# Performance work log

Hardware: AMD Instinct MI355X
Metric: run time of the kernel (lower is better)

The kernel has to match this reference:

```python
import jax, jax.numpy as jnp
import numpy as np

E = 64; H = 4; DQK = 1; B = 2; R = 1225; C = 512; EPS_LN = 1e-5


def _ln(x, g, b):
    m = x.mean(-1, keepdims=True)
    v = jnp.mean((x - m) ** 2, -1, keepdims=True)
    return (x - m) / jnp.sqrt(v + EPS_LN) * g + b


def _lin_attn(x, wq, bq, wk, bk, wv, bv, wo, bo):
    # x: (b, r, c, e); attention over axis c (nb_col), per head, ELU+1 feature map
    b_, r_, c_, e_ = x.shape
    dv = e_ // H
    q = (x @ wq.T + bq).reshape(b_, r_, c_, H, DQK).swapaxes(2, 3)  # (b,r,H,c,dqk)
    k = (x @ wk.T + bk).reshape(b_, r_, c_, H, DQK).swapaxes(2, 3)
    v = (x @ wv.T + bv).reshape(b_, r_, c_, H, dv).swapaxes(2, 3)   # (b,r,H,c,dv)
    q = jax.nn.elu(q) + 1.0
    k = jax.nn.elu(k) + 1.0
    q = q / q.mean(axis=3, keepdims=True)  # mean over seq (c)
    k = k / k.sum(axis=3, keepdims=True)   # sum over seq (c)
    ktv = jnp.einsum('brhcd,brhce->brhde', k, v)   # (b,r,H,dqk,dv)
    o = jnp.einsum('brhcd,brhde->brhce', q, ktv)   # (b,r,H,c,dv)
    o = o.swapaxes(2, 3).reshape(b_, r_, c_, e_)
    return o @ wo.T + bo


def setup_inputs():
    key = jax.random.key(0)
    ks = iter(jax.random.split(key, 32))
    def w(shape, s=0.05):
        return jax.random.normal(next(ks), shape, jnp.float32) * s
    inp = {"x": jax.random.normal(next(ks), (B, E, R, C), jnp.float32)}
    for p in ("row", "col"):
        inp[p + "_wq"] = w((H, E)); inp[p + "_bq"] = jnp.zeros((H,), jnp.float32)
        inp[p + "_wk"] = w((H, E)); inp[p + "_bk"] = jnp.zeros((H,), jnp.float32)
        inp[p + "_wv"] = w((E, E)); inp[p + "_bv"] = jnp.zeros((E,), jnp.float32)
        inp[p + "_wo"] = w((E, E)); inp[p + "_bo"] = jnp.zeros((E,), jnp.float32)
    for p in ("rn", "cn", "fn"):
        inp[p + "_g"] = jnp.ones((E,), jnp.float32)
        inp[p + "_b"] = jnp.zeros((E,), jnp.float32)
    inp["w1"] = w((4 * E, E)); inp["b1"] = jnp.zeros((4 * E,), jnp.float32)
    inp["w2"] = w((E, 4 * E)); inp["b2"] = jnp.zeros((E,), jnp.float32)
    return inp


def reference(x, row_wq, row_bq, row_wk, row_bk, row_wv, row_bv, row_wo, row_bo,
              col_wq, col_bq, col_wk, col_bk, col_wv, col_bv, col_wo, col_bo,
              rn_g, rn_b, cn_g, cn_b, fn_g, fn_b, w1, b1, w2, b2):
    xe = jnp.moveaxis(x, 1, -1)  # (B, R, C, E)
    # row attention: attend over cols (C)
    h = xe + _lin_attn(_ln(xe, rn_g, rn_b),
                       row_wq, row_bq, row_wk, row_bk, row_wv, row_bv, row_wo, row_bo)
    # col attention: attend over rows (R) -> swap axes
    hc = _ln(h.swapaxes(1, 2), cn_g, cn_b)  # (B, C, R, E)
    h = h + _lin_attn(hc, col_wq, col_bq, col_wk, col_bk, col_wv, col_bv, col_wo, col_bo).swapaxes(1, 2)
    # 1x1-conv FFN == per-position MLP with exact GELU
    f = _ln(h, fn_g, fn_b)
    f = jax.nn.gelu(f @ w1.T + b1, approximate=False) @ w2.T + b2
    return jnp.moveaxis(h + f, -1, 1)  # (B, E, R, C)
```

## Files before the change

kernel.cpp:

```cpp
#include <hip/hip_runtime.h>
#include <cmath>

#define E_ 64
#define H_ 4
#define B_ 2
#define R_ 1225
#define C_ 512
#define EPS 1e-5f

__device__ __forceinline__ float elu1(float a) { return a > 0.f ? a + 1.f : __expf(a); }

typedef float f32x4 __attribute__((ext_vector_type(4)));
typedef short bf16x8 __attribute__((ext_vector_type(8)));
typedef short bf16x4 __attribute__((ext_vector_type(4)));

__device__ __forceinline__ unsigned short f2bf(float f) {
    union { float f; unsigned u; } c; c.f = f;
    unsigned u = c.u + 0x7FFFu + ((c.u >> 16) & 1u);
    return (unsigned short)(u >> 16);
}

__device__ __forceinline__ unsigned short f2bf_rn(float f) {
    union { float f; unsigned u; } c; c.f = f;
    return (unsigned short)((c.u + 0x8000u) >> 16);
}

__device__ __forceinline__ float bf2f(unsigned short s) {
    union { unsigned u; float f; } c; c.u = ((unsigned)s) << 16;
    return c.f;
}

__device__ __forceinline__ float gelu_fast(float a) {
    const float u = a * (-1.5957691216057308f - 0.0713548162726009f * a * a);
    return a / (1.f + __expf(u));
}


#define SXR 520

__global__ __launch_bounds__(512, 2) void row_attn(
    const float* __restrict__ x,
    const float* __restrict__ wq, const float* __restrict__ bq,
    const float* __restrict__ wk, const float* __restrict__ bk,
    const float* __restrict__ wv, const float* __restrict__ bv,
    const float* __restrict__ wo, const float* __restrict__ bo,
    const float* __restrict__ lng, const float* __restrict__ lnb,
    short* __restrict__ hout)
{
    const int r = blockIdx.x;
    const int b = blockIdx.y;
    const int t = threadIdx.x;
    const int w = t >> 6;
    const int l = t & 63;
    const int lr = l & 15;
    const int lq = l >> 4;

    __shared__ short s_xT[E_][SXR];
    __shared__ short s_kb[4][SXR];
    __shared__ float s_upart[2][H_][E_];
    __shared__ float s_ktv[E_];
    __shared__ float s_wok[E_][H_];
    __shared__ float s_qm[H_];
    __shared__ float s_sk[H_];
    __shared__ float s_S1[H_];
    __shared__ float red_q[8][H_];
    __shared__ float red_k[8][H_];
    __shared__ float red_k2[8][H_];
    __shared__ float s_cst[16];

    if (t < 16) {
        const int h = t & 3;
        const int kind = t >> 2;
        const float* wm = (kind < 2) ? wq : wk;
        const float* vm = (kind & 1) ? lnb : lng;
        float acc = 0.f;
        for (int e = 0; e < E_; ++e) acc += wm[h * E_ + e] * vm[e];
        s_cst[t] = acc;
    }
    __syncthreads();

    const size_t RC = (size_t)R_ * C_;
    const float* xbase = x + (size_t)b * E_ * RC + (size_t)r * C_;

    float qs[H_];
    float aq[H_], ak[H_], ak2[H_];
    {
        const float* xp = xbase + t;
        float s = 0.f, ss = 0.f;
        float dq[H_] = {0.f, 0.f, 0.f, 0.f};
        float dk[H_] = {0.f, 0.f, 0.f, 0.f};
        #pragma unroll 16
        for (int e = 0; e < E_; ++e) {
            const float xv = xp[(size_t)e * RC];
            s += xv; ss += xv * xv;
            const float t1 = lng[e] * xv;
            #pragma unroll
            for (int h = 0; h < H_; ++h) { dq[h] += wq[h * E_ + e] * t1; dk[h] += wk[h * E_ + e] * t1; }
            s_xT[e][t] = (short)f2bf(xv);
        }
        const float mu = s * (1.f / E_);
        const float rstd = rsqrtf(ss * (1.f / E_) - mu * mu + EPS);
        const float mr = mu * rstd;
        #pragma unroll
        for (int h = 0; h < H_; ++h) {
            const float qv = elu1(rstd * dq[h] - mr * s_cst[h]     + s_cst[4 + h]  + bq[h]);
            const float kv = elu1(rstd * dk[h] - mr * s_cst[8 + h] + s_cst[12 + h] + bk[h]);
            qs[h] = qv;
            aq[h] = qv; ak[h] = kv; ak2[h] = kv * mr;
            s_kb[h][t] = (short)f2bf(kv * rstd);
        }
    }
    __syncthreads();

    {
        const int et = w & 3;
        const int kh = w >> 2;
        f32x4 uacc; uacc[0] = uacc[1] = uacc[2] = uacc[3] = 0.f;
        #pragma unroll
        for (int ks = 0; ks < 8; ++ks) {
            const int co = kh * 256 + ks * 32 + lq * 8;
            bf16x8 af;
            #pragma unroll
            for (int i = 0; i < 8; ++i) af[i] = 0;
            if (lr < 4) af = *reinterpret_cast<const bf16x8*>(&s_kb[lr][co]);
            const bf16x8 bf = *reinterpret_cast<const bf16x8*>(&s_xT[et * 16 + lr][co]);
            uacc = __builtin_amdgcn_mfma_f32_16x16x32_bf16(af, bf, uacc, 0, 0, 0);
        }
        if (lq == 0) {
            #pragma unroll
            for (int i = 0; i < 4; ++i) s_upart[kh][i][et * 16 + lr] = uacc[i];
        }
    }

    #pragma unroll
    for (int h = 0; h < H_; ++h) {
        #pragma unroll
        for (int off = 32; off; off >>= 1) {
            aq[h] += __shfl_xor(aq[h], off, 64);
            ak[h] += __shfl_xor(ak[h], off, 64);
            ak2[h] += __shfl_xor(ak2[h], off, 64);
        }
    }
    if (l == 0) {
        #pragma unroll
        for (int h = 0; h < H_; ++h) { red_q[w][h] = aq[h]; red_k[w][h] = ak[h]; red_k2[w][h] = ak2[h]; }
    }
    __syncthreads();
    if (t < H_) {
        float sq = 0.f, sk = 0.f, s1 = 0.f;
        #pragma unroll
        for (int w2 = 0; w2 < 8; ++w2) { sq += red_q[w2][t]; sk += red_k[w2][t]; s1 += red_k2[w2][t]; }
        s_qm[t] = sq * (1.f / C_);
        s_sk[t] = sk;
        s_S1[t] = s1;
    }
    __syncthreads();
    if (t < H_ * E_) {
        const int h = t >> 6, e = t & 63;
        const float m1 = s_upart[0][h][e] + s_upart[1][h][e];
        s_upart[0][h][e] = lng[e] * (m1 - s_S1[h]) + lnb[e] * s_sk[h];
    }
    __syncthreads();
    if (t < E_) {
        const int h = t >> 4;
        float acc = 0.f;
        #pragma unroll
        for (int e = 0; e < E_; ++e) acc += wv[t * E_ + e] * s_upart[0][h][e];
        s_ktv[t] = acc / s_sk[h] + bv[t];
    }
    __syncthreads();
    if (t < E_) {
        #pragma unroll
        for (int h = 0; h < H_; ++h) {
            float acc = 0.f;
            #pragma unroll
            for (int d = 0; d < 16; ++d) acc += wo[t * E_ + h * 16 + d] * s_ktv[h * 16 + d];
            s_wok[t][h] = acc;
        }
    }
    __syncthreads();

    {
        float qn[H_];
        #pragma unroll
        for (int h = 0; h < H_; ++h) qn[h] = qs[h] / s_qm[h];
        short* hp = hout + ((size_t)((size_t)b * R_ + r) * C_ + t) * E_;
        #pragma unroll
        for (int e8 = 0; e8 < 8; ++e8) {
            bf16x8 o;
            #pragma unroll
            for (int i = 0; i < 8; ++i) {
                const int e = e8 * 8 + i;
                float tt = bo[e];
                #pragma unroll
                for (int h = 0; h < H_; ++h) tt += qn[h] * s_wok[e][h];
                o[i] = (short)f2bf(bf2f((unsigned short)s_xT[e][t]) + tt);
            }
            *reinterpret_cast<bf16x8*>(hp + e8 * 8) = o;
        }
    }
}

#define SX 264

__global__ __launch_bounds__(256, 3) void col_stats(
    const short* __restrict__ hbuf,
    const float* __restrict__ wq, const float* __restrict__ bq,
    const float* __restrict__ wk, const float* __restrict__ bk,
    const float* __restrict__ wv, const float* __restrict__ bv,
    const float* __restrict__ wo,
    const float* __restrict__ lng, const float* __restrict__ lnb,
    unsigned short* __restrict__ qbuf, float* __restrict__ wokq)
{
    const int c = blockIdx.x;
    const int b = blockIdx.y;
    const int t = threadIdx.x;
    const int w = t >> 6;
    const int l = t & 63;
    const int lr = l & 15;
    const int lq = l >> 4;

    __shared__ short s_xT[E_][SX];
    __shared__ short s_kb[4][SX];
    __shared__ float s_u[H_][E_];
    __shared__ float s_ktv[E_];
    __shared__ float s_wok[E_][H_];
    __shared__ float s_qm[H_];
    __shared__ float s_sk[H_];
    __shared__ float s_S1[H_];
    __shared__ float red_q[4][H_];
    __shared__ float red_k[4][H_];
    __shared__ float red_k2[4][H_];
    __shared__ float s_cst[16];

    if (t < 16) {
        const int h = t & 3;
        const int kind = t >> 2;
        const float* wm = (kind < 2) ? wq : wk;
        const float* vm = (kind & 1) ? lnb : lng;
        float acc = 0.f;
        for (int e = 0; e < E_; ++e) acc += wm[h * E_ + e] * vm[e];
        s_cst[t] = acc;
    }
    __syncthreads();

    const size_t CE = (size_t)C_ * E_;
    const short* hp0 = hbuf + (size_t)b * R_ * CE + (size_t)c * E_;
    unsigned short* qb0 = qbuf + ((size_t)(b * C_ + c)) * R_ * 4;

    float aq[H_]  = {0.f, 0.f, 0.f, 0.f};
    float ak[H_]  = {0.f, 0.f, 0.f, 0.f};
    float ak2[H_] = {0.f, 0.f, 0.f, 0.f};
    f32x4 uacc; uacc[0] = uacc[1] = uacc[2] = uacc[3] = 0.f;

    #pragma unroll 1
    for (int it = 0; it < 5; ++it) {
        const int rr = it * 256 + t;
        if (rr < R_) {
            const short* pp = hp0 + (size_t)rr * CE;
            bf16x8 hv8[8];
            #pragma unroll
            for (int g = 0; g < 8; ++g) hv8[g] = *reinterpret_cast<const bf16x8*>(pp + g * 8);
            float s = 0.f, ss = 0.f;
            float dq[H_] = {0.f, 0.f, 0.f, 0.f};
            float dk[H_] = {0.f, 0.f, 0.f, 0.f};
            #pragma unroll
            for (int g = 0; g < 8; ++g) {
                #pragma unroll
                for (int i = 0; i < 8; ++i) {
                    const int e = g * 8 + i;
                    const float xv = bf2f((unsigned short)hv8[g][i]);
                    s += xv; ss += xv * xv;
                    const float t1 = lng[e] * xv;
                    #pragma unroll
                    for (int h = 0; h < H_; ++h) { dq[h] += wq[h * E_ + e] * t1; dk[h] += wk[h * E_ + e] * t1; }
                    s_xT[e][t] = hv8[g][i];
                }
            }
            const float mu = s * (1.f / E_);
            const float rstd = rsqrtf(ss * (1.f / E_) - mu * mu + EPS);
            const float mr = mu * rstd;
            float qv[H_];
            #pragma unroll
            for (int h = 0; h < H_; ++h) {
                qv[h] = elu1(rstd * dq[h] - mr * s_cst[h]     + s_cst[4 + h]  + bq[h]);
                const float kv = elu1(rstd * dk[h] - mr * s_cst[8 + h] + s_cst[12 + h] + bk[h]);
                aq[h] += qv[h]; ak[h] += kv; ak2[h] += kv * mr;
                s_kb[h][t] = (short)f2bf(kv * rstd);
            }
            uint2 qp;
            qp.x = ((unsigned)f2bf(qv[1]) << 16) | f2bf(qv[0]);
            qp.y = ((unsigned)f2bf(qv[3]) << 16) | f2bf(qv[2]);
            *reinterpret_cast<uint2*>(qb0 + (size_t)rr * 4) = qp;
        } else {
            #pragma unroll
            for (int e = 0; e < E_; ++e) s_xT[e][t] = 0;
            #pragma unroll
            for (int h = 0; h < H_; ++h) s_kb[h][t] = 0;
        }
        __syncthreads();
        #pragma unroll
        for (int ks = 0; ks < 8; ++ks) {
            bf16x8 af;
            #pragma unroll
            for (int i = 0; i < 8; ++i) af[i] = 0;
            if (lr < 4) af = *reinterpret_cast<const bf16x8*>(&s_kb[lr][ks * 32 + lq * 8]);
            const bf16x8 bf = *reinterpret_cast<const bf16x8*>(&s_xT[w * 16 + lr][ks * 32 + lq * 8]);
            uacc = __builtin_amdgcn_mfma_f32_16x16x32_bf16(af, bf, uacc, 0, 0, 0);
        }
        __syncthreads();
    }

    #pragma unroll
    for (int h = 0; h < H_; ++h) {
        #pragma unroll
        for (int off = 32; off; off >>= 1) {
            aq[h] += __shfl_xor(aq[h], off, 64);
            ak[h] += __shfl_xor(ak[h], off, 64);
            ak2[h] += __shfl_xor(ak2[h], off, 64);
        }
    }
    if (l == 0) {
        #pragma unroll
        for (int h = 0; h < H_; ++h) { red_q[w][h] = aq[h]; red_k[w][h] = ak[h]; red_k2[w][h] = ak2[h]; }
    }
    __syncthreads();
    if (t < H_) {
        float sq = 0.f, sk = 0.f, s1 = 0.f;
        #pragma unroll
        for (int w2 = 0; w2 < 4; ++w2) { sq += red_q[w2][t]; sk += red_k[w2][t]; s1 += red_k2[w2][t]; }
        s_qm[t] = sq * (1.f / R_);
        s_sk[t] = sk;
        s_S1[t] = s1;
    }
    __syncthreads();
    if (lq == 0) {
        const int e = w * 16 + lr;
        #pragma unroll
        for (int i = 0; i < 4; ++i)
            s_u[i][e] = lng[e] * (uacc[i] - s_S1[i]) + lnb[e] * s_sk[i];
    }
    __syncthreads();
    if (t < E_) {
        const int h = t >> 4;
        float acc = 0.f;
        #pragma unroll
        for (int e = 0; e < E_; ++e) acc += wv[t * E_ + e] * s_u[h][e];
        s_ktv[t] = acc / s_sk[h] + bv[t];
    }
    __syncthreads();
    if (t < E_) {
        #pragma unroll
        for (int h = 0; h < H_; ++h) {
            float acc = 0.f;
            #pragma unroll
            for (int d = 0; d < 16; ++d) acc += wo[t * E_ + h * 16 + d] * s_ktv[h * 16 + d];
            s_wok[t][h] = acc;
        }
    }
    __syncthreads();

    {
        const int e = t >> 2, h = t & 3;
        wokq[((size_t)(b * C_ + c)) * 256 + t] = s_wok[e][h] / s_qm[h];
    }
}

__global__ __launch_bounds__(256) void prep_weights(
    const float* __restrict__ w1, const float* __restrict__ w2,
    short* __restrict__ w1b, short* __restrict__ w2b)
{
    const int i = blockIdx.x * 256 + threadIdx.x;
    if (i < 16384) w1b[i] = (short)f2bf(w1[i]);
    else           w2b[i - 16384] = (short)f2bf(w2[i - 16384]);
}

#define SA 72
#define SG 264
#define SO 68

#define SWZS(row, col) ((col) ^ (((row) & 7) << 3))
#define SWZF(row, col) ((col) ^ (((row) & 7) << 2))

__global__ __launch_bounds__(256) void ffn_mfma(
    const short* __restrict__ hbuf,
    const unsigned short* __restrict__ qbuf, const float* __restrict__ wokq,
    const float* __restrict__ cbo,
    const float* __restrict__ lng, const float* __restrict__ lnb,
    const short* __restrict__ w1b, const float* __restrict__ b1,
    const short* __restrict__ w2b, const float* __restrict__ b2,
    float* __restrict__ out)
{
    __shared__ __align__(16) char smem[33792 + 17408];
    short* s_g = (short*)smem;
    short* s_a = (short*)(smem + 33792);
    float* s_o = (float*)(smem + 33792);
    float* s_ln = (float*)(smem + 43008);

    const int t = threadIdx.x;
    const int w = t >> 6;
    const int l = t & 63;
    const int lr = l & 15;
    const int lq = l >> 4;

    const int bid = blockIdx.x;
    const int cb  = bid & 7;
    const int rem = bid >> 3;
    const int r   = rem % R_;
    const int b   = rem / R_;
    const int c0  = cb * 64;

    const short* tile = hbuf + ((size_t)((size_t)b * R_ + r) * C_ + c0) * E_;

    const int m  = l;
    const int eb = w * 16;
    float hc[16];
    {
        const short* hp = tile + (size_t)m * E_ + eb;
        const bf16x8 v0 = *reinterpret_cast<const bf16x8*>(hp);
        const bf16x8 v1 = *reinterpret_cast<const bf16x8*>(hp + 8);
        const uint2 qp = *reinterpret_cast<const uint2*>(
            qbuf + ((size_t)(b * C_ + c0 + m) * R_ + r) * 4);
        float qv[4];
        qv[0] = bf2f((unsigned short)(qp.x & 0xFFFF));
        qv[1] = bf2f((unsigned short)(qp.x >> 16));
        qv[2] = bf2f((unsigned short)(qp.y & 0xFFFF));
        qv[3] = bf2f((unsigned short)(qp.y >> 16));
        const float4* wq4 = reinterpret_cast<const float4*>(
            wokq + ((size_t)(b * C_ + c0 + m)) * 256) + eb;
        float s = 0.f, ss = 0.f;
        #pragma unroll
        for (int i = 0; i < 16; ++i) {
            const int e = eb + i;
            const float4 f4 = wq4[i];
            const float hv = bf2f((unsigned short)(i < 8 ? v0[i] : v1[i - 8]));
            hc[i] = hv + cbo[e] + qv[0] * f4.x + qv[1] * f4.y + qv[2] * f4.z + qv[3] * f4.w;
            s += hc[i]; ss += hc[i] * hc[i];
        }
        s_ln[w * 64 + m]       = s;
        s_ln[256 + w * 64 + m] = ss;
    }
    __syncthreads();

    {
        const float s  = s_ln[m] + s_ln[64 + m] + s_ln[128 + m] + s_ln[192 + m];
        const float ss = s_ln[256 + m] + s_ln[320 + m] + s_ln[384 + m] + s_ln[448 + m];
        const float mu = s * (1.f / 64.f);
        const float rstd = rsqrtf(ss * (1.f / 64.f) - mu * mu + EPS);
        bf16x8 o0, o1;
        #pragma unroll
        for (int i = 0; i < 8; ++i) {
            const int e = eb + i;
            o0[i] = (short)f2bf_rn((hc[i] - mu) * rstd * lng[e] + lnb[e]);
        }
        #pragma unroll
        for (int i = 0; i < 8; ++i) {
            const int e = eb + 8 + i;
            o1[i] = (short)f2bf_rn((hc[8 + i] - mu) * rstd * lng[e] + lnb[e]);
        }
        *reinterpret_cast<bf16x8*>(&s_a[m * SA + SWZS(m, eb)])     = o0;
        *reinterpret_cast<bf16x8*>(&s_a[m * SA + SWZS(m, eb + 8)]) = o1;
    }
    __syncthreads();

    {
        bf16x8 bfr[4][2];
        #pragma unroll
        for (int mt = 0; mt < 4; ++mt) {
            const int row = mt * 16 + lr;
            #pragma unroll
            for (int ks = 0; ks < 2; ++ks)
                bfr[mt][ks] = *reinterpret_cast<const bf16x8*>(
                    &s_a[row * SA + SWZS(row, ks * 32 + lq * 8)]);
        }

        #pragma unroll
        for (int nn = 0; nn < 4; ++nn) {
            const int jt = w * 4 + nn;
            bf16x8 afr[2];
            #pragma unroll
            for (int ks = 0; ks < 2; ++ks)
                afr[ks] = *reinterpret_cast<const bf16x8*>(
                    w1b + (size_t)(jt * 16 + lr) * 64 + ks * 32 + lq * 8);
            f32x4 acc[4];
            #pragma unroll
            for (int mt = 0; mt < 4; ++mt) { acc[mt][0]=0.f; acc[mt][1]=0.f; acc[mt][2]=0.f; acc[mt][3]=0.f; }
            #pragma unroll
            for (int ks = 0; ks < 2; ++ks)
                #pragma unroll
                for (int mt = 0; mt < 4; ++mt)
                    acc[mt] = __builtin_amdgcn_mfma_f32_16x16x32_bf16(afr[ks], bfr[mt][ks], acc[mt], 0, 0, 0);

            const float4 b1v = *reinterpret_cast<const float4*>(&b1[jt * 16 + lq * 4]);
            const float* b1p = (const float*)&b1v;
            #pragma unroll
            for (int mt = 0; mt < 4; ++mt) {
                const int mm = mt * 16 + lr;
                bf16x4 pk;
                #pragma unroll
                for (int i = 0; i < 4; ++i) {
                    const float aa = acc[mt][i] + b1p[i];
                    pk[i] = (short)f2bf_rn(gelu_fast(aa));
                }
                *reinterpret_cast<bf16x4*>(&s_g[mm * SG + SWZS(mm, jt * 16 + lq * 4)]) = pk;
            }
        }
    }
    __syncthreads();

    {
        f32x4 acc2[4];
        #pragma unroll
        for (int mt = 0; mt < 4; ++mt) { acc2[mt][0]=0.f; acc2[mt][1]=0.f; acc2[mt][2]=0.f; acc2[mt][3]=0.f; }
        const int n = w * 16 + lr;
        #pragma unroll
        for (int ks = 0; ks < 8; ++ks) {
            const bf16x8 bfr = *reinterpret_cast<const bf16x8*>(
                w2b + (size_t)n * 256 + ks * 32 + lq * 8);
            #pragma unroll
            for (int mt = 0; mt < 4; ++mt) {
                const int row = mt * 16 + lr;
                const bf16x8 af = *reinterpret_cast<const bf16x8*>(
                    &s_g[row * SG + SWZS(row, ks * 32 + lq * 8)]);
                acc2[mt] = __builtin_amdgcn_mfma_f32_16x16x32_bf16(af, bfr, acc2[mt], 0, 0, 0);
            }
        }
        #pragma unroll
        for (int mt = 0; mt < 4; ++mt)
            #pragma unroll
            for (int i = 0; i < 4; ++i) {
                const int row = mt * 16 + lq * 4 + i;
                s_o[row * SO + SWZF(row, n)] = acc2[mt][i];
            }
    }
    __syncthreads();

    {
        const size_t RC = (size_t)R_ * C_;
        float* op = out + (size_t)b * E_ * RC + (size_t)r * C_ + (c0 + m);
        #pragma unroll
        for (int j = 0; j < 4; ++j) {
            const float4 so4 = *reinterpret_cast<const float4*>(
                &s_o[m * SO + SWZF(m, eb + j * 4)]);
            const float* sop = (const float*)&so4;
            #pragma unroll
            for (int i = 0; i < 4; ++i) {
                const int e = eb + j * 4 + i;
                op[(size_t)e * RC] = hc[j * 4 + i] + b2[e] + sop[i];
            }
        }
    }
}

extern "C" void kernel_launch(void* const* d_in, const int* in_sizes, int n_in,
                              void* d_out, int out_size, void* d_ws, size_t ws_size,
                              hipStream_t stream) {
    const float* x      = (const float*)d_in[0];
    const float* row_wq = (const float*)d_in[1];
    const float* row_bq = (const float*)d_in[2];
    const float* row_wk = (const float*)d_in[3];
    const float* row_bk = (const float*)d_in[4];
    const float* row_wv = (const float*)d_in[5];
    const float* row_bv = (const float*)d_in[6];
    const float* row_wo = (const float*)d_in[7];
    const float* row_bo = (const float*)d_in[8];
    const float* col_wq = (const float*)d_in[9];
    const float* col_bq = (const float*)d_in[10];
    const float* col_wk = (const float*)d_in[11];
    const float* col_bk = (const float*)d_in[12];
    const float* col_wv = (const float*)d_in[13];
    const float* col_bv = (const float*)d_in[14];
    const float* col_wo = (const float*)d_in[15];
    const float* col_bo = (const float*)d_in[16];
    const float* rn_g   = (const float*)d_in[17];
    const float* rn_b   = (const float*)d_in[18];
    const float* cn_g   = (const float*)d_in[19];
    const float* cn_b   = (const float*)d_in[20];
    const float* fn_g   = (const float*)d_in[21];
    const float* fn_b   = (const float*)d_in[22];
    const float* w1     = (const float*)d_in[23];
    const float* b1     = (const float*)d_in[24];
    const float* w2     = (const float*)d_in[25];
    const float* b2     = (const float*)d_in[26];

    const size_t n_h   = (size_t)B_ * R_ * C_ * E_;
    const size_t n_q   = (size_t)B_ * C_ * R_ * 4;
    const size_t n_wok = (size_t)B_ * C_ * 256;
    const size_t need  = n_h * 2 + n_q * 2 + n_wok * 4 + 2 * 16384 * 2;
    if (ws_size < need) return;

    short* hbuf = (short*)d_ws;
    unsigned short* qbuf = (unsigned short*)(hbuf + n_h);
    float* wokq = (float*)(qbuf + n_q);
    short* w1b = (short*)(wokq + n_wok);
    short* w2b = w1b + 16384;

    row_attn<<<dim3(R_, B_), 512, 0, stream>>>(
        x, row_wq, row_bq, row_wk, row_bk, row_wv, row_bv, row_wo, row_bo,
        rn_g, rn_b, hbuf);
    prep_weights<<<128, 256, 0, stream>>>(w1, w2, w1b, w2b);
    col_stats<<<dim3(C_, B_), 256, 0, stream>>>(
        hbuf, col_wq, col_bq, col_wk, col_bk, col_wv, col_bv, col_wo,
        cn_g, cn_b, qbuf, wokq);
    ffn_mfma<<<B_ * R_ * 8, 256, 0, stream>>>(
        hbuf, qbuf, wokq, col_bo, fn_g, fn_b, w1b, b1, w2b, b2, (float*)d_out);
}
```

Baseline: 731.1 us.

## Split FFN hidden dimension into two halves to shrink shared memory

The FFN kernel now computes the 256-wide GELU hidden layer in two 128-wide halves. Each half goes through a smaller shared buffer and is accumulated into the second GEMM before the next half is produced. This cuts the LDS footprint from about 50KB to 28KB so more blocks can be resident per CU, at the cost of extra barriers. The XOR swizzles on the shared arrays are also removed in favour of plain padded strides, which may bring back some bank conflicts.

```diff
diff --git a/kernel.cpp b/kernel.cpp
--- a/kernel.cpp
+++ b/kernel.cpp
@@ -376,11 +376,8 @@
 }
 
 #define SA 72
-#define SG 264
+#define SGH 136
 #define SO 68
-
-#define SWZS(row, col) ((col) ^ (((row) & 7) << 3))
-#define SWZF(row, col) ((col) ^ (((row) & 7) << 2))
 
 __global__ __launch_bounds__(256) void ffn_mfma(
     const short* __restrict__ hbuf,
@@ -391,11 +388,11 @@
     const short* __restrict__ w2b, const float* __restrict__ b2,
     float* __restrict__ out)
 {
-    __shared__ __align__(16) char smem[33792 + 17408];
-    short* s_g = (short*)smem;
-    short* s_a = (short*)(smem + 33792);
-    float* s_o = (float*)(smem + 33792);
-    float* s_ln = (float*)(smem + 43008);
+    __shared__ __align__(16) char smem[28672];
+    short* s_a = (short*)smem;
+    short* s_g = (short*)(smem + 9216);
+    float* s_o = (float*)(smem + 9216);
+    float* s_ln = (float*)(smem + 26624);
 
     const int t = threadIdx.x;
     const int w = t >> 6;
@@ -458,30 +455,35 @@
             const int e = eb + 8 + i;
             o1[i] = (short)f2bf_rn((hc[8 + i] - mu) * rstd * lng[e] + lnb[e]);
         }
-        *reinterpret_cast<bf16x8*>(&s_a[m * SA + SWZS(m, eb)])     = o0;
-        *reinterpret_cast<bf16x8*>(&s_a[m * SA + SWZS(m, eb + 8)]) = o1;
-    }
-    __syncthreads();
-
-    {
-        bf16x8 bfr[4][2];
-        #pragma unroll
-        for (int mt = 0; mt < 4; ++mt) {
-            const int row = mt * 16 + lr;
-            #pragma unroll
-            for (int ks = 0; ks < 2; ++ks)
-                bfr[mt][ks] = *reinterpret_cast<const bf16x8*>(
-                    &s_a[row * SA + SWZS(row, ks * 32 + lq * 8)]);
-        }
-
-        #pragma unroll
-        for (int nn = 0; nn < 4; ++nn) {
-            const int jt = w * 4 + nn;
+        *reinterpret_cast<bf16x8*>(&s_a[m * SA + eb])     = o0;
+        *reinterpret_cast<bf16x8*>(&s_a[m * SA + eb + 8]) = o1;
+    }
+    __syncthreads();
+
+    bf16x8 bfr[4][2];
+    #pragma unroll
+    for (int mt = 0; mt < 4; ++mt)
+        #pragma unroll
+        for (int ks = 0; ks < 2; ++ks)
+            bfr[mt][ks] = *reinterpret_cast<const bf16x8*>(
+                &s_a[(mt * 16 + lr) * SA + ks * 32 + lq * 8]);
+
+    f32x4 acc2[4];
+    #pragma unroll
+    for (int mt = 0; mt < 4; ++mt) { acc2[mt][0]=0.f; acc2[mt][1]=0.f; acc2[mt][2]=0.f; acc2[mt][3]=0.f; }
+    const int n = w * 16 + lr;
+
+    #pragma unroll
+    for (int hh = 0; hh < 2; ++hh) {
+        #pragma unroll
+        for (int nn = 0; nn < 2; ++nn) {
+            const int jtl = w * 2 + nn;
+            const int jg  = (hh << 7) + jtl * 16;
             bf16x8 afr[2];
             #pragma unroll
             for (int ks = 0; ks < 2; ++ks)
                 afr[ks] = *reinterpret_cast<const bf16x8*>(
-                    w1b + (size_t)(jt * 16 + lr) * 64 + ks * 32 + lq * 8);
+                    w1b + (size_t)(jg + lr) * 64 + ks * 32 + lq * 8);
             f32x4 acc[4];
             #pragma unroll
             for (int mt = 0; mt < 4; ++mt) { acc[mt][0]=0.f; acc[mt][1]=0.f; acc[mt][2]=0.f; acc[mt][3]=0.f; }
@@ -491,7 +493,7 @@
                 for (int mt = 0; mt < 4; ++mt)
                     acc[mt] = __builtin_amdgcn_mfma_f32_16x16x32_bf16(afr[ks], bfr[mt][ks], acc[mt], 0, 0, 0);
 
-            const float4 b1v = *reinterpret_cast<const float4*>(&b1[jt * 16 + lq * 4]);
+            const float4 b1v = *reinterpret_cast<const float4*>(&b1[jg + lq * 4]);
             const float* b1p = (const float*)&b1v;
             #pragma unroll
             for (int mt = 0; mt < 4; ++mt) {
@@ -502,36 +504,31 @@
                     const float aa = acc[mt][i] + b1p[i];
                     pk[i] = (short)f2bf_rn(gelu_fast(aa));
                 }
-                *reinterpret_cast<bf16x4*>(&s_g[mm * SG + SWZS(mm, jt * 16 + lq * 4)]) = pk;
+                *reinterpret_cast<bf16x4*>(&s_g[mm * SGH + jtl * 16 + lq * 4]) = pk;
             }
         }
-    }
-    __syncthreads();
-
-    {
-        f32x4 acc2[4];
-        #pragma unroll
-        for (int mt = 0; mt < 4; ++mt) { acc2[mt][0]=0.f; acc2[mt][1]=0.f; acc2[mt][2]=0.f; acc2[mt][3]=0.f; }
-        const int n = w * 16 + lr;
-        #pragma unroll
-        for (int ks = 0; ks < 8; ++ks) {
-            const bf16x8 bfr = *reinterpret_cast<const bf16x8*>(
-                w2b + (size_t)n * 256 + ks * 32 + lq * 8);
+        __syncthreads();
+
+        #pragma unroll
+        for (int ks = 0; ks < 4; ++ks) {
+            const bf16x8 bf2v = *reinterpret_cast<const bf16x8*>(
+                w2b + (size_t)n * 256 + (hh << 7) + ks * 32 + lq * 8);
             #pragma unroll
             for (int mt = 0; mt < 4; ++mt) {
-                const int row = mt * 16 + lr;
                 const bf16x8 af = *reinterpret_cast<const bf16x8*>(
-                    &s_g[row * SG + SWZS(row, ks * 32 + lq * 8)]);
-                acc2[mt] = __builtin_amdgcn_mfma_f32_16x16x32_bf16(af, bfr, acc2[mt], 0, 0, 0);
+                    &s_g[(mt * 16 + lr) * SGH + ks * 32 + lq * 8]);
+                acc2[mt] = __builtin_amdgcn_mfma_f32_16x16x32_bf16(af, bf2v, acc2[mt], 0, 0, 0);
             }
         }
+        __syncthreads();
+    }
+
+    {
         #pragma unroll
         for (int mt = 0; mt < 4; ++mt)
             #pragma unroll
-            for (int i = 0; i < 4; ++i) {
-                const int row = mt * 16 + lq * 4 + i;
-                s_o[row * SO + SWZF(row, n)] = acc2[mt][i];
-            }
+            for (int i = 0; i < 4; ++i)
+                s_o[(mt * 16 + lq * 4 + i) * SO + n] = acc2[mt][i];
     }
     __syncthreads();
 
@@ -541,7 +538,7 @@
         #pragma unroll
         for (int j = 0; j < 4; ++j) {
             const float4 so4 = *reinterpret_cast<const float4*>(
-                &s_o[m * SO + SWZF(m, eb + j * 4)]);
+                &s_o[m * SO + eb + j * 4]);
             const float* sop = (const float*)&so4;
             #pragma unroll
             for (int i = 0; i < 4; ++i) {
```

Result: no change. 742.7 us (+1.6%).
